# Kernel optimization log

Hardware: AMD Instinct MI355X
Metric: run time of the kernel (lower is better)

## Reference

```python
import jax, jax.numpy as jnp
import numpy as np

D_MODEL = 1024
HEADS = 16
Q_DIM = 1024
HEAD_DIM = Q_DIM // HEADS


def setup_inputs() -> dict:
    key = jax.random.key(0)
    ks = jax.random.split(key, 9)
    B, S = 2, 2048
    scale = 1.0 / np.sqrt(D_MODEL)
    inp = {
        "embeddings": jax.random.normal(ks[0], (B, S, D_MODEL), dtype=jnp.float32),
        "Wq": jax.random.normal(ks[1], (D_MODEL, Q_DIM), dtype=jnp.float32) * scale,
        "bq": jnp.zeros((Q_DIM,), dtype=jnp.float32),
        "Wk": jax.random.normal(ks[2], (D_MODEL, Q_DIM), dtype=jnp.float32) * scale,
        "bk": jnp.zeros((Q_DIM,), dtype=jnp.float32),
        "Wv": jax.random.normal(ks[3], (D_MODEL, Q_DIM), dtype=jnp.float32) * scale,
        "bv": jnp.zeros((Q_DIM,), dtype=jnp.float32),
        "Wo": jax.random.normal(ks[4], (Q_DIM, D_MODEL), dtype=jnp.float32) * scale,
        "bo": jnp.zeros((D_MODEL,), dtype=jnp.float32),
    }
    return inp


def reference(embeddings, Wq, bq, Wk, bk, Wv, bv, Wo, bo):
    B, S, _ = embeddings.shape
    # projections -> [B, H, S, Dh]
    def proj(W, b):
        x = embeddings @ W + b
        return x.reshape(B, S, HEADS, HEAD_DIM).transpose(0, 2, 1, 3)
    q = proj(Wq, bq)
    k = proj(Wk, bk)
    v = proj(Wv, bv)
    # scores scaled by sqrt(head_dim) as in source (no mask, dropout is no-op)
    scores = jnp.einsum("bhqd,bhkd->bhqk", q, k) / jnp.sqrt(
        jnp.asarray(HEAD_DIM, dtype=q.dtype)
    )
    p = jax.nn.softmax(scores, axis=-1)
    attn = jnp.einsum("bhqk,bhkd->bhqd", p, v)
    attn = attn.transpose(0, 2, 1, 3).reshape(B, S, Q_DIM)
    return attn @ Wo + bo
```

## Files before the change

### kernel.cpp

```cpp
#include <hip/hip_runtime.h>
#include <hip/hip_bf16.h>

#define BB 2
#define SS 2048
#define DMODEL 1024
#define NHEADS 16
#define DHEAD 64
#define MTOT (BB*SS)
#define NQKV 3072
#define QSCALE 0.18033688011112042f

typedef short bh8 __attribute__((ext_vector_type(8)));
typedef float fx4 __attribute__((ext_vector_type(4)));
typedef unsigned int ux2 __attribute__((ext_vector_type(2)));

__device__ __forceinline__ short f2bs(float f) {
    __hip_bfloat16 h = __float2bfloat16(f);
    return *reinterpret_cast<short*>(&h);
}

__device__ __forceinline__ unsigned pk_bf16(float a, float b) {
    __hip_bfloat162 h = __float22bfloat162_rn(make_float2(a, b));
    return *reinterpret_cast<unsigned*>(&h);
}

__device__ __forceinline__ void gload_lds16(const short* g, short* l) {
    __builtin_amdgcn_global_load_lds(
        (const __attribute__((address_space(1))) unsigned int*)g,
        (__attribute__((address_space(3))) unsigned int*)l, 16, 0, 0);
}

__global__ __launch_bounds__(256) void cvt_emb(const float* __restrict__ x,
                                               short* __restrict__ y, int n) {
    int i = (blockIdx.x * 256 + threadIdx.x) * 4;
    if (i + 3 < n) {
        float4 v = *(const float4*)(x + i);
        short4 o;
        o.x = f2bs(v.x); o.y = f2bs(v.y); o.z = f2bs(v.z); o.w = f2bs(v.w);
        *(short4*)(y + i) = o;
    }
}

__global__ __launch_bounds__(256) void transpose_w(
        const float* __restrict__ Wq, const float* __restrict__ Wk,
        const float* __restrict__ Wv, const float* __restrict__ Wo,
        short* __restrict__ Wt_qkv, short* __restrict__ Wot) {
    __shared__ float tile[64][65];
    int z = blockIdx.z;
    const float* src = (z == 0) ? Wq : (z == 1) ? Wk : (z == 2) ? Wv : Wo;
    short* dst = (z == 3) ? Wot : (Wt_qkv + (size_t)z * 1024 * 1024);
    int n0 = blockIdx.x * 64, k0 = blockIdx.y * 64;
    int tx = threadIdx.x, ty = threadIdx.y;
    for (int j = 0; j < 16; j++) {
        int r = ty + j * 4;
        tile[r][tx] = src[(size_t)(k0 + r) * 1024 + n0 + tx];
    }
    __syncthreads();
    for (int j = 0; j < 16; j++) {
        int r = ty + j * 4;
        dst[(size_t)(n0 + r) * 1024 + k0 + tx] = f2bs(tile[tx][r]);
    }
}

template<int BM, int BN, int NN, int MODE>
__global__ __launch_bounds__(256) void gemm_bt_t(
        const short* __restrict__ A, const short* __restrict__ Bt,
        const float* __restrict__ bq, const float* __restrict__ bk,
        const float* __restrict__ bv, const float* __restrict__ bo,
        short* __restrict__ Qout, short* __restrict__ Kout,
        short* __restrict__ Vtout, float* __restrict__ Cout) {
    const int K = 1024;
    constexpr int ROWS = BM + BN;
    constexpr int CPW  = ROWS / 64;
    constexpr int MBK  = MTOT / BM;
    constexpr int STRIP = MBK / 8;
    constexpr int MT = BM / 32, NT = BN / 32;
    __shared__ __align__(16) short S[3][ROWS * 32];

    int tid = threadIdx.x;
    int w = tid >> 6, l = tid & 63, quad = l >> 4, ln = l & 15;
    int wm = w & 1, wn = w >> 1;

    int id = blockIdx.x;
    int xcd = id & 7, local = id >> 3;
    int mi = xcd * STRIP + (local % STRIP);
    int ni = local / STRIP;
    int m0 = mi * BM, n0 = ni * BN;

    const short* gsrc[CPW];
    int loff[CPW];
    #pragma unroll
    for (int j = 0; j < CPW; j++) {
        int r0 = (w * CPW + j) * 16;
        int row = r0 + (l >> 2);
        gsrc[j] = (r0 < BM ? A + (size_t)(m0 + row) * K
                           : Bt + (size_t)(n0 + row - BM) * K) + (l & 3) * 8;
        loff[j] = r0 * 32;
    }

    short *sC = &S[0][0], *sN = &S[1][0], *sN2 = &S[2][0];
    #pragma unroll
    for (int j = 0; j < CPW; j++) gload_lds16(gsrc[j], sC + loff[j]);
    #pragma unroll
    for (int j = 0; j < CPW; j++) gload_lds16(gsrc[j] + 32, sN + loff[j]);

    fx4 acc[MT][NT] = {};
    for (int it = 0; it < 32; ++it) {
        if (it < 31) {
            if constexpr (CPW == 4)
                asm volatile("s_waitcnt vmcnt(4)\n\ts_barrier" ::: "memory");
            else
                asm volatile("s_waitcnt vmcnt(3)\n\ts_barrier" ::: "memory");
        } else {
            asm volatile("s_waitcnt vmcnt(0)\n\ts_barrier" ::: "memory");
        }
        if (it < 30) {
            int k0 = (it + 2) * 32;
            #pragma unroll
            for (int j = 0; j < CPW; j++) gload_lds16(gsrc[j] + k0, sN2 + loff[j]);
        }
        bh8 af[MT], bf[NT];
        #pragma unroll
        for (int mt = 0; mt < MT; mt++)
            af[mt] = *(const bh8*)&sC[(wm * (BM / 2) + mt * 16 + ln) * 32 + quad * 8];
        #pragma unroll
        for (int nt = 0; nt < NT; nt++)
            bf[nt] = *(const bh8*)&sC[(BM + wn * (BN / 2) + nt * 16 + ln) * 32 + quad * 8];
        #pragma unroll
        for (int mt = 0; mt < MT; mt++)
            #pragma unroll
            for (int nt = 0; nt < NT; nt++)
                acc[mt][nt] = __builtin_amdgcn_mfma_f32_16x16x32_bf16(af[mt], bf[nt], acc[mt][nt], 0, 0, 0);
        short* t;
        t = sC; sC = sN; sN = sN2; sN2 = t;
    }

    #pragma unroll
    for (int mt = 0; mt < MT; mt++) {
        #pragma unroll
        for (int nt = 0; nt < NT; nt++) {
            int n = n0 + wn * (BN / 2) + nt * 16 + ln;
            int mbase = m0 + wm * (BM / 2) + mt * 16 + quad * 4;
            #pragma unroll
            for (int r = 0; r < 4; r++) {
                float v = acc[mt][nt][r];
                int m = mbase + r;
                if constexpr (MODE == 0) {
                    int which = n >> 10, nn = n & 1023, h = nn >> 6, d = nn & 63;
                    float bias = (which == 0) ? bq[nn] : (which == 1) ? bk[nn] : bv[nn];
                    v += bias;
                    int b = m >> 11, s = m & 2047;
                    if (which == 0)
                        Qout[(((size_t)(b * 16 + h) * 2048) + s) * 64 + d] = f2bs(v * QSCALE);
                    else if (which == 1)
                        Kout[(((size_t)(b * 16 + h) * 2048) + s) * 64 + d] = f2bs(v);
                    else
                        Vtout[((size_t)(b * 16 + h) * 64 + d) * 2048 + s] = f2bs(v);
                } else {
                    Cout[(size_t)m * 1024 + n] = v + bo[n];
                }
            }
        }
    }
}

__global__ __launch_bounds__(256, 4) void flash_attn(
        const short* __restrict__ Q, const short* __restrict__ Kg,
        const short* __restrict__ Vt, short* __restrict__ Ctx) {
    __shared__ __align__(16) short SH[16384];

    int tid = threadIdx.x;
    int w = tid >> 6, l = tid & 63, quad = l >> 4, ln = l & 15;
    int wq = w & 1, wk = w >> 1;
    int id = blockIdx.x;
    int xcd = id & 7, local = id >> 3;
    int bh = xcd * 4 + (local & 3);
    int qx = local >> 2;
    int qblk = qx * 64 + wq * 32;
    int b = bh >> 4, h = bh & 15;
    const short* Qb = Q  + (size_t)bh * 2048 * 64;
    const short* Kb = Kg + (size_t)bh * 2048 * 64;
    const short* Vb = Vt + (size_t)bh * 64 * 2048;
    int swz = ln & 7;

    bh8 qf[2][2];
    #pragma unroll
    for (int qt = 0; qt < 2; qt++)
        #pragma unroll
        for (int c = 0; c < 2; c++)
            qf[qt][c] = *(const bh8*)&Qb[(size_t)(qblk + qt * 16 + ln) * 64 + c * 32 + quad * 8];

    union { short s[8]; bh8 v; } one_;
    #pragma unroll
    for (int j = 0; j < 8; j++) one_.s[j] = 0x3F80;
    bh8 onesv = one_.v;

    const short* srcK[2]; const short* srcV[2]; int dstoff[2];
    #pragma unroll
    for (int j = 0; j < 2; j++) {
        int c = w * 2 + j;
        int row = c * 8 + (l >> 3);
        int pg = (l & 7) ^ (row & 7);
        srcK[j] = Kb + row * 64 + pg * 8;
        srcV[j] = Vb + (size_t)row * 2048 + pg * 8;
        dstoff[j] = c * 512;
    }

    #pragma unroll
    for (int j = 0; j < 2; j++) {
        gload_lds16(srcK[j], SH + dstoff[j]);
        gload_lds16(srcV[j], SH + 8192 + dstoff[j]);
    }

    fx4 o[2][4] = {};
    fx4 lacc[2] = {};

    for (int it = 0; it < 32; ++it) {
        int koff = (it & 1) ? 4096 : 0;
        asm volatile("s_waitcnt vmcnt(0) lgkmcnt(0)\n\ts_barrier" ::: "memory");
        if (it < 31) {
            int noff = koff ^ 4096;
            int kg = (it + 1) * 4096, vg = (it + 1) * 64;
            #pragma unroll
            for (int j = 0; j < 2; j++) {
                gload_lds16(srcK[j] + kg, SH + noff + dstoff[j]);
                gload_lds16(srcV[j] + vg, SH + 8192 + noff + dstoff[j]);
            }
        }
        const short* ksb = SH + koff;
        const short* vsb = SH + 8192 + koff;

        bh8 kf[2][2];
        #pragma unroll
        for (int mt = 0; mt < 2; mt++) {
            int krow = (wk * 32 + mt * 16 + ln) * 64;
            kf[mt][0] = *(const bh8*)&ksb[krow + ((quad ^ swz) * 8)];
            kf[mt][1] = *(const bh8*)&ksb[krow + (((quad + 4) ^ swz) * 8)];
        }
        fx4 s[2][2] = {};
        __builtin_amdgcn_s_setprio(1);
        #pragma unroll
        for (int mt = 0; mt < 2; mt++)
            #pragma unroll
            for (int qt = 0; qt < 2; qt++) {
                s[qt][mt] = __builtin_amdgcn_mfma_f32_16x16x32_bf16(kf[mt][0], qf[qt][0], s[qt][mt], 0, 0, 0);
                s[qt][mt] = __builtin_amdgcn_mfma_f32_16x16x32_bf16(kf[mt][1], qf[qt][1], s[qt][mt], 0, 0, 0);
            }
        __builtin_amdgcn_s_setprio(0);

        bh8 pf[2];
        #pragma unroll
        for (int qt = 0; qt < 2; qt++) {
            float e0[4], e1[4];
            #pragma unroll
            for (int r = 0; r < 4; r++) {
                e0[r] = __builtin_amdgcn_exp2f(s[qt][0][r]);
                e1[r] = __builtin_amdgcn_exp2f(s[qt][1][r]);
            }
            unsigned xa = pk_bf16(e0[0], e0[1]);
            unsigned ya = pk_bf16(e0[2], e0[3]);
            unsigned xb = pk_bf16(e1[0], e1[1]);
            unsigned yb = pk_bf16(e1[2], e1[3]);
            ux2 u   = __builtin_amdgcn_permlane32_swap(xa, xb, false, false);
            ux2 d02 = __builtin_amdgcn_permlane16_swap(u.x, u.y, false, false);
            ux2 u2  = __builtin_amdgcn_permlane32_swap(ya, yb, false, false);
            ux2 d13 = __builtin_amdgcn_permlane16_swap(u2.x, u2.y, false, false);
            union { unsigned u4[4]; bh8 v; } pk_;
            pk_.u4[0] = d02.x; pk_.u4[1] = d13.x;
            pk_.u4[2] = d02.y; pk_.u4[3] = d13.y;
            pf[qt] = pk_.v;
        }

        __builtin_amdgcn_s_setprio(1);
        #pragma unroll
        for (int dt = 0; dt < 4; dt++) {
            bh8 vf = *(const bh8*)&vsb[(dt * 16 + ln) * 64 + (((wk * 4 + quad) ^ swz) * 8)];
            o[0][dt] = __builtin_amdgcn_mfma_f32_16x16x32_bf16(vf, pf[0], o[0][dt], 0, 0, 0);
            o[1][dt] = __builtin_amdgcn_mfma_f32_16x16x32_bf16(vf, pf[1], o[1][dt], 0, 0, 0);
        }
        lacc[0] = __builtin_amdgcn_mfma_f32_16x16x32_bf16(onesv, pf[0], lacc[0], 0, 0, 0);
        lacc[1] = __builtin_amdgcn_mfma_f32_16x16x32_bf16(onesv, pf[1], lacc[1], 0, 0, 0);
        __builtin_amdgcn_s_setprio(0);
    }

    asm volatile("s_waitcnt vmcnt(0) lgkmcnt(0)\n\ts_barrier" ::: "memory");

    float* R  = (float*)SH + 2176;
    float* R2 = (float*)SH + 2176 + 4096;

    if (wk == 1) {
        float* Rw = R + wq * 2048;
        #pragma unroll
        for (int qt = 0; qt < 2; qt++)
            #pragma unroll
            for (int dt = 0; dt < 4; dt++)
                *(fx4*)&Rw[(((qt * 4 + dt) * 4 + quad) * 16 + ln) * 4] = o[qt][dt];
        if (quad == 0) {
            R2[wq * 32 + 0 * 16 + ln] = lacc[0][0];
            R2[wq * 32 + 1 * 16 + ln] = lacc[1][0];
        }
    }
    asm volatile("s_waitcnt lgkmcnt(0)\n\ts_barrier" ::: "memory");

    if (wk == 0) {
        float* Rw = R + wq * 2048;
        float linv[2];
        #pragma unroll
        for (int qt = 0; qt < 2; qt++) {
            #pragma unroll
            for (int dt = 0; dt < 4; dt++)
                o[qt][dt] += *(const fx4*)&Rw[(((qt * 4 + dt) * 4 + quad) * 16 + ln) * 4];
            float lf = lacc[qt][0] + R2[wq * 32 + qt * 16 + ln];
            linv[qt] = 1.0f / lf;
        }
        float* PsF = (float*)SH + wq * 1088;
        int row = l >> 2, seg = l & 3;
        #pragma unroll
        for (int qt = 0; qt < 2; qt++) {
            #pragma unroll
            for (int dt = 0; dt < 4; dt++)
                *(fx4*)&PsF[ln * 68 + dt * 16 + quad * 4] = o[qt][dt];
            asm volatile("s_waitcnt lgkmcnt(0)" ::: "memory");
            float invr = __shfl(linv[qt], row);
            int q = qblk + qt * 16 + row;
            short* crow = Ctx + ((size_t)(b * 2048 + q)) * 1024 + h * 64 + seg * 16;
            union { short s[8]; uint4 u; } o0, o1;
            #pragma unroll
            for (int j = 0; j < 2; j++) {
                fx4 v = *(const fx4*)&PsF[row * 68 + seg * 16 + j * 4];
                o0.s[j * 4 + 0] = f2bs(v[0] * invr);
                o0.s[j * 4 + 1] = f2bs(v[1] * invr);
                o0.s[j * 4 + 2] = f2bs(v[2] * invr);
                o0.s[j * 4 + 3] = f2bs(v[3] * invr);
            }
            #pragma unroll
            for (int j = 2; j < 4; j++) {
                fx4 v = *(const fx4*)&PsF[row * 68 + seg * 16 + j * 4];
                o1.s[(j - 2) * 4 + 0] = f2bs(v[0] * invr);
                o1.s[(j - 2) * 4 + 1] = f2bs(v[1] * invr);
                o1.s[(j - 2) * 4 + 2] = f2bs(v[2] * invr);
                o1.s[(j - 2) * 4 + 3] = f2bs(v[3] * invr);
            }
            *(uint4*)&crow[0] = o0.u;
            *(uint4*)&crow[8] = o1.u;
            asm volatile("s_waitcnt lgkmcnt(0)" ::: "memory");
        }
    }
}

extern "C" void kernel_launch(void* const* d_in, const int* in_sizes, int n_in,
                              void* d_out, int out_size, void* d_ws, size_t ws_size,
                              hipStream_t stream) {
    const float* emb = (const float*)d_in[0];
    const float* Wq  = (const float*)d_in[1];
    const float* bq  = (const float*)d_in[2];
    const float* Wk  = (const float*)d_in[3];
    const float* bk  = (const float*)d_in[4];
    const float* Wv  = (const float*)d_in[5];
    const float* bv  = (const float*)d_in[6];
    const float* Wo  = (const float*)d_in[7];
    const float* bo  = (const float*)d_in[8];

    char* ws = (char*)d_ws;
    const size_t MB = 1024 * 1024;
    short* Xbf  = (short*)(ws + 0);
    short* Ctx  = (short*)(ws + 0);
    short* Wt   = (short*)(ws + 8 * MB);
    short* Wot  = (short*)(ws + 17 * MB);
    short* Qb   = (short*)(ws + 19 * MB);
    short* Kb   = (short*)(ws + 27 * MB);
    short* Vtb  = (short*)(ws + 35 * MB);

    cvt_emb<<<4096, 256, 0, stream>>>(emb, Xbf, MTOT * DMODEL);
    transpose_w<<<dim3(16, 16, 4), dim3(64, 4), 0, stream>>>(Wq, Wk, Wv, Wo, Wt, Wot);
    gemm_bt_t<128, 128, NQKV, 0><<<768, 256, 0, stream>>>(
        Xbf, Wt, bq, bk, bv, nullptr, Qb, Kb, Vtb, nullptr);
    flash_attn<<<1024, 256, 0, stream>>>(Qb, Kb, Vtb, Ctx);
    gemm_bt_t<64, 128, DMODEL, 1><<<512, 256, 0, stream>>>(
        Ctx, Wot, nullptr, nullptr, nullptr, bo, nullptr, nullptr, nullptr, (float*)d_out);
}
```

Before: 198.9 us.

## Fuse prep kernels and vectorize QKV GEMM epilogue stores via LDS and permlane

```diff
diff --git a/kernel.cpp b/kernel.cpp
--- a/kernel.cpp
+++ b/kernel.cpp
@@ -30,35 +30,35 @@
         (__attribute__((address_space(3))) unsigned int*)l, 16, 0, 0);
 }
 
-__global__ __launch_bounds__(256) void cvt_emb(const float* __restrict__ x,
-                                               short* __restrict__ y, int n) {
-    int i = (blockIdx.x * 256 + threadIdx.x) * 4;
-    if (i + 3 < n) {
-        float4 v = *(const float4*)(x + i);
-        short4 o;
-        o.x = f2bs(v.x); o.y = f2bs(v.y); o.z = f2bs(v.z); o.w = f2bs(v.w);
-        *(short4*)(y + i) = o;
-    }
-}
-
-__global__ __launch_bounds__(256) void transpose_w(
+__global__ __launch_bounds__(256) void prep(
+        const float* __restrict__ emb, short* __restrict__ Xbf,
         const float* __restrict__ Wq, const float* __restrict__ Wk,
         const float* __restrict__ Wv, const float* __restrict__ Wo,
         short* __restrict__ Wt_qkv, short* __restrict__ Wot) {
     __shared__ float tile[64][65];
-    int z = blockIdx.z;
-    const float* src = (z == 0) ? Wq : (z == 1) ? Wk : (z == 2) ? Wv : Wo;
-    short* dst = (z == 3) ? Wot : (Wt_qkv + (size_t)z * 1024 * 1024);
-    int n0 = blockIdx.x * 64, k0 = blockIdx.y * 64;
-    int tx = threadIdx.x, ty = threadIdx.y;
-    for (int j = 0; j < 16; j++) {
-        int r = ty + j * 4;
-        tile[r][tx] = src[(size_t)(k0 + r) * 1024 + n0 + tx];
-    }
-    __syncthreads();
-    for (int j = 0; j < 16; j++) {
-        int r = ty + j * 4;
-        dst[(size_t)(n0 + r) * 1024 + k0 + tx] = f2bs(tile[tx][r]);
+    int bid = blockIdx.x, tid = threadIdx.x;
+    if (bid < 4096) {
+        int i = (bid * 256 + tid) * 4;
+        float4 v = *(const float4*)(emb + i);
+        short4 o;
+        o.x = f2bs(v.x); o.y = f2bs(v.y); o.z = f2bs(v.z); o.w = f2bs(v.w);
+        *(short4*)(Xbf + i) = o;
+    } else {
+        int b2 = bid - 4096;
+        int bx = b2 & 15, by = (b2 >> 4) & 15, z = b2 >> 8;
+        const float* src = (z == 0) ? Wq : (z == 1) ? Wk : (z == 2) ? Wv : Wo;
+        short* dst = (z == 3) ? Wot : (Wt_qkv + (size_t)z * 1024 * 1024);
+        int n0 = bx * 64, k0 = by * 64;
+        int tx = tid & 63, ty = tid >> 6;
+        for (int j = 0; j < 16; j++) {
+            int r = ty + j * 4;
+            tile[r][tx] = src[(size_t)(k0 + r) * 1024 + n0 + tx];
+        }
+        __syncthreads();
+        for (int j = 0; j < 16; j++) {
+            int r = ty + j * 4;
+            dst[(size_t)(n0 + r) * 1024 + k0 + tx] = f2bs(tile[tx][r]);
+        }
     }
 }
 
@@ -87,6 +87,9 @@
     int ni = local / STRIP;
     int m0 = mi * BM, n0 = ni * BN;
 
+    const int which = (MODE == 0) ? (n0 >> 10) : 2;
+    const bool swp = (MODE == 0) && (which != 2);
+
     const short* gsrc[CPW];
     int loff[CPW];
     #pragma unroll
@@ -126,38 +129,113 @@
         #pragma unroll
         for (int nt = 0; nt < NT; nt++)
             bf[nt] = *(const bh8*)&sC[(BM + wn * (BN / 2) + nt * 16 + ln) * 32 + quad * 8];
-        #pragma unroll
-        for (int mt = 0; mt < MT; mt++)
-            #pragma unroll
-            for (int nt = 0; nt < NT; nt++)
-                acc[mt][nt] = __builtin_amdgcn_mfma_f32_16x16x32_bf16(af[mt], bf[nt], acc[mt][nt], 0, 0, 0);
+        if (!swp) {
+            #pragma unroll
+            for (int mt = 0; mt < MT; mt++)
+                #pragma unroll
+                for (int nt = 0; nt < NT; nt++)
+                    acc[mt][nt] = __builtin_amdgcn_mfma_f32_16x16x32_bf16(af[mt], bf[nt], acc[mt][nt], 0, 0, 0);
+        } else {
+            #pragma unroll
+            for (int mt = 0; mt < MT; mt++)
+                #pragma unroll
+                for (int nt = 0; nt < NT; nt++)
+                    acc[mt][nt] = __builtin_amdgcn_mfma_f32_16x16x32_bf16(bf[nt], af[mt], acc[mt][nt], 0, 0, 0);
+        }
         short* t;
         t = sC; sC = sN; sN = sN2; sN2 = t;
     }
 
-    #pragma unroll
-    for (int mt = 0; mt < MT; mt++) {
-        #pragma unroll
-        for (int nt = 0; nt < NT; nt++) {
-            int n = n0 + wn * (BN / 2) + nt * 16 + ln;
-            int mbase = m0 + wm * (BM / 2) + mt * 16 + quad * 4;
-            #pragma unroll
-            for (int r = 0; r < 4; r++) {
-                float v = acc[mt][nt][r];
-                int m = mbase + r;
-                if constexpr (MODE == 0) {
-                    int which = n >> 10, nn = n & 1023, h = nn >> 6, d = nn & 63;
-                    float bias = (which == 0) ? bq[nn] : (which == 1) ? bk[nn] : bv[nn];
-                    v += bias;
-                    int b = m >> 11, s = m & 2047;
-                    if (which == 0)
-                        Qout[(((size_t)(b * 16 + h) * 2048) + s) * 64 + d] = f2bs(v * QSCALE);
-                    else if (which == 1)
-                        Kout[(((size_t)(b * 16 + h) * 2048) + s) * 64 + d] = f2bs(v);
-                    else
-                        Vtout[((size_t)(b * 16 + h) * 64 + d) * 2048 + s] = f2bs(v);
-                } else {
-                    Cout[(size_t)m * 1024 + n] = v + bo[n];
+    if constexpr (MODE == 0) {
+        int nbase = n0 + wn * 64;
+        int nn0 = nbase & 1023;
+        int h = nn0 >> 6;
+        int mbase_w = m0 + wm * 64;
+        int bb_ = mbase_w >> 11, s0 = mbase_w & 2047;
+
+        if (which == 2) {
+            #pragma unroll
+            for (int nt = 0; nt < NT; nt++) {
+                float bias = bv[nn0 + nt * 16 + ln];
+                #pragma unroll
+                for (int mt = 0; mt < MT; mt++)
+                    #pragma unroll
+                    for (int r = 0; r < 4; r++)
+                        acc[mt][nt][r] += bias;
+            }
+            #pragma unroll
+            for (int nt = 0; nt < NT; nt++) {
+                int d = nt * 16 + ln;
+                short* vrow = Vtout + ((size_t)(bb_ * 16 + h) * 64 + d) * 2048 + s0;
+                #pragma unroll
+                for (int mp = 0; mp < MT / 2; mp++) {
+                    fx4 ea = acc[2 * mp][nt], eb = acc[2 * mp + 1][nt];
+                    unsigned xa = pk_bf16(ea[0], ea[1]);
+                    unsigned ya = pk_bf16(ea[2], ea[3]);
+                    unsigned xb = pk_bf16(eb[0], eb[1]);
+                    unsigned yb = pk_bf16(eb[2], eb[3]);
+                    ux2 u   = __builtin_amdgcn_permlane32_swap(xa, xb, false, false);
+                    ux2 d02 = __builtin_amdgcn_permlane16_swap(u.x, u.y, false, false);
+                    ux2 u2  = __builtin_amdgcn_permlane32_swap(ya, yb, false, false);
+                    ux2 d13 = __builtin_amdgcn_permlane16_swap(u2.x, u2.y, false, false);
+                    union { unsigned u4[4]; uint4 v; } pk_;
+                    pk_.u4[0] = d02.x; pk_.u4[1] = d13.x;
+                    pk_.u4[2] = d02.y; pk_.u4[3] = d13.y;
+                    *(uint4*)(vrow + (mp * 32 + quad * 8)) = pk_.v;
+                }
+            }
+        } else {
+            const float* bptr = (which == 0) ? bq : bk;
+            float scl = (which == 0) ? QSCALE : 1.0f;
+            short* out = (which == 0) ? Qout : Kout;
+            asm volatile("s_waitcnt lgkmcnt(0)\n\ts_barrier" ::: "memory");
+            float* PsF = (float*)&S[0][0] + w * 1088;
+            int row = l >> 2, seg = l & 3;
+            fx4 bjv[4];
+            #pragma unroll
+            for (int j = 0; j < 4; j++)
+                bjv[j] = *(const fx4*)&bptr[nn0 + seg * 16 + j * 4];
+            #pragma unroll
+            for (int mt = 0; mt < MT; mt++) {
+                #pragma unroll
+                for (int nt = 0; nt < NT; nt++)
+                    *(fx4*)&PsF[ln * 68 + nt * 16 + quad * 4] = acc[mt][nt];
+                asm volatile("s_waitcnt lgkmcnt(0)" ::: "memory");
+                int s_ = s0 + mt * 16 + row;
+                short* crow = out + (((size_t)(bb_ * 16 + h) * 2048) + s_) * 64 + seg * 16;
+                union { short sv[8]; uint4 u; } o0, o1;
+                #pragma unroll
+                for (int j = 0; j < 2; j++) {
+                    fx4 v = *(const fx4*)&PsF[row * 68 + seg * 16 + j * 4];
+                    o0.sv[j * 4 + 0] = f2bs((v[0] + bjv[j][0]) * scl);
+                    o0.sv[j * 4 + 1] = f2bs((v[1] + bjv[j][1]) * scl);
+                    o0.sv[j * 4 + 2] = f2bs((v[2] + bjv[j][2]) * scl);
+                    o0.sv[j * 4 + 3] = f2bs((v[3] + bjv[j][3]) * scl);
+                }
+                #pragma unroll
+                for (int j = 2; j < 4; j++) {
+                    fx4 v = *(const fx4*)&PsF[row * 68 + seg * 16 + j * 4];
+                    o1.sv[(j - 2) * 4 + 0] = f2bs((v[0] + bjv[j][0]) * scl);
+                    o1.sv[(j - 2) * 4 + 1] = f2bs((v[1] + bjv[j][1]) * scl);
+                    o1.sv[(j - 2) * 4 + 2] = f2bs((v[2] + bjv[j][2]) * scl);
+                    o1.sv[(j - 2) * 4 + 3] = f2bs((v[3] + bjv[j][3]) * scl);
+                }
+                *(uint4*)&crow[0] = o0.u;
+                *(uint4*)&crow[8] = o1.u;
+                asm volatile("s_waitcnt lgkmcnt(0)" ::: "memory");
+            }
+        }
+    } else {
+        #pragma unroll
+        for (int mt = 0; mt < MT; mt++) {
+            #pragma unroll
+            for (int nt = 0; nt < NT; nt++) {
+                int n = n0 + wn * (BN / 2) + nt * 16 + ln;
+                int mbase = m0 + wm * (BM / 2) + mt * 16 + quad * 4;
+                #pragma unroll
+                for (int r = 0; r < 4; r++) {
+                    int m = mbase + r;
+                    Cout[(size_t)m * 1024 + n] = acc[mt][nt][r] + bo[n];
                 }
             }
         }
@@ -371,8 +449,7 @@
     short* Kb   = (short*)(ws + 27 * MB);
     short* Vtb  = (short*)(ws + 35 * MB);
 
-    cvt_emb<<<4096, 256, 0, stream>>>(emb, Xbf, MTOT * DMODEL);
-    transpose_w<<<dim3(16, 16, 4), dim3(64, 4), 0, stream>>>(Wq, Wk, Wv, Wo, Wt, Wot);
+    prep<<<5120, 256, 0, stream>>>(emb, Xbf, Wq, Wk, Wv, Wo, Wt, Wot);
     gemm_bt_t<128, 128, NQKV, 0><<<768, 256, 0, stream>>>(
         Xbf, Wt, bq, bk, bv, nullptr, Qb, Kb, Vtb, nullptr);
     flash_attn<<<1024, 256, 0, stream>>>(Qb, Kb, Vtb, Ctx);
```

After: 198.3 us. Within noise of the previous version (-0.3%).
